# Kernel optimization log

Hardware: AMD Instinct MI355X
Metric: run time of the kernel (lower is better)

The kernel has to match this reference:

```python
import jax, jax.numpy as jnp
import numpy as np

EPS = 1e-8  # torch F.cosine_similarity default eps

N, M, PLANES = 4096, 4096, 512


def setup_inputs() -> dict:
    key = jax.random.key(0)
    k1, k2, k3, k4 = jax.random.split(key, 4)
    pre = jax.random.normal(k1, (N, PLANES), dtype=jnp.float32)
    cur = jax.random.normal(k2, (M, PLANES), dtype=jnp.float32)
    adj = jax.random.uniform(k3, (N, M), dtype=jnp.float32)
    stdv = 1.0 / np.sqrt(PLANES)
    weight = jax.random.uniform(k4, (PLANES, PLANES), dtype=jnp.float32,
                                minval=-stdv, maxval=stdv)
    return {"pre": pre, "cur": cur, "adj": adj, "weight": weight}


def reference(pre, cur, adj, weight):
    # --- GraphConvolution ---
    pre_w = pre @ weight            # [N, P]
    cur_w = cur @ weight            # [M, P]
    pre_h = adj @ cur_w             # [N, P]  adj_norm @ cur_
    cur_h = adj.T @ pre_w           # [M, P]  adj_t_norm @ pre_

    # --- edge_update: tan(cosine_similarity) for all (i, j) pairs, fused ---
    # cosine_similarity(x, y) = (x . y) / (max(||x||, eps) * max(||y||, eps))
    pre_norm = jnp.maximum(jnp.linalg.norm(pre_h, axis=1, keepdims=True), EPS)
    cur_norm = jnp.maximum(jnp.linalg.norm(cur_h, axis=1, keepdims=True), EPS)
    pre_n = pre_h / pre_norm        # [N, P]
    cur_n = cur_h / cur_norm        # [M, P]
    cos = pre_n @ cur_n.T           # [N, M]
    adj_out = jnp.tan(cos)          # [N, M]
    score = adj_out.reshape(-1)     # [N*M], row-major == i * M + j ordering
    return (score, adj_out)
```

## Files before the change

### kernel.cpp

```cpp
#include <hip/hip_runtime.h>

typedef unsigned short ushort_t;
typedef __attribute__((ext_vector_type(8))) short short8;
typedef __attribute__((ext_vector_type(4))) float f32x4;

__device__ __forceinline__ ushort_t f2bf(float x) {
  union { float f; unsigned u; } v; v.f = x;
  unsigned r = v.u + 0x7fffu + ((v.u >> 16) & 1u);
  return (ushort_t)(r >> 16);
}
__device__ __forceinline__ float bf2f(ushort_t h) {
  union { unsigned u; float f; } v; v.u = ((unsigned)h) << 16;
  return v.f;
}

__device__ __forceinline__ void async_cp16(const ushort_t* g, ushort_t* lds) {
  __builtin_amdgcn_global_load_lds(
      (const __attribute__((address_space(1))) unsigned int*)g,
      (__attribute__((address_space(3))) unsigned int*)lds, 16, 0, 0);
}

template <int MT, int NT, int BKT, int EPI>
__device__ __forceinline__ void gemm_core2(
    const ushort_t* __restrict__ A, int lda,
    const ushort_t* __restrict__ B, int ldb,
    int K,
    ushort_t* sA, ushort_t* sB,
    ushort_t* Cb, float* Cf0, float* Cf1, int ldc,
    const float* __restrict__ ip, const float* __restrict__ ic) {
  constexpr int MI = MT / 32, NI = NT / 32, KU = BKT / 32;
  constexpr int LPR = BKT / 8;
  constexpr int RPC = 256 / LPR;
  constexpr int ASZ = MT * BKT, BSZ = NT * BKT;
  static_assert(LPR == 8, "swizzle assumes 8 segs per row");
  static_assert(RPC % 8 == 0, "row&7 must be per-lane constant");
  const int t = threadIdx.x;
  const int wave = t >> 6, lane = t & 63;
  const int lm = lane & 15, lq = lane >> 4;
  const int wr = wave >> 1, wc = wave & 1;

  f32x4 acc[MI][NI] = {};

  const int srow = t / LPR;
  const int gseg = (t % LPR) ^ (srow & 7);
  const ushort_t* ga = A + (size_t)srow * lda + gseg * 8;
  const ushort_t* gb = B + (size_t)srow * ldb + gseg * 8;
  const int sw = lm & 7;

  auto stage = [&](int k0, int buf) {
    ushort_t* dA = sA + buf * ASZ + wave * 512;
    ushort_t* dB = sB + buf * BSZ + wave * 512;
#pragma unroll
    for (int j = 0; j < MT / RPC; j++)
      async_cp16(ga + k0 + (size_t)j * RPC * lda, dA + j * 2048);
#pragma unroll
    for (int j = 0; j < NT / RPC; j++)
      async_cp16(gb + k0 + (size_t)j * RPC * ldb, dB + j * 2048);
  };

  stage(0, 0);
  int cur = 0;
  for (int k0 = 0; k0 < K; k0 += BKT) {
    __syncthreads();
    if (k0 + BKT < K) stage(k0 + BKT, cur ^ 1);
    const ushort_t* cA = sA + cur * ASZ;
    const ushort_t* cB = sB + cur * BSZ;
#pragma unroll
    for (int ku = 0; ku < KU; ku++) {
      short8 af[MI], bf4[NI];
#pragma unroll
      for (int i = 0; i < MI; i++)
        af[i] = *(const short8*)(cA + (wr * (MT / 2) + i * 16 + lm) * BKT +
                                 ((ku * 4 + lq) ^ sw) * 8);
#pragma unroll
      for (int i = 0; i < NI; i++)
        bf4[i] = *(const short8*)(cB + (wc * (NT / 2) + i * 16 + lm) * BKT +
                                  ((ku * 4 + lq) ^ sw) * 8);
#pragma unroll
      for (int mt = 0; mt < MI; mt++)
#pragma unroll
        for (int nt = 0; nt < NI; nt++)
          acc[mt][nt] = __builtin_amdgcn_mfma_f32_16x16x32_bf16(
              af[mt], bf4[nt], acc[mt][nt], 0, 0, 0);
    }
    cur ^= 1;
  }

#pragma unroll
  for (int mt = 0; mt < MI; mt++) {
    int rb = wr * (MT / 2) + mt * 16 + lq * 4;
#pragma unroll
    for (int nt = 0; nt < NI; nt++) {
      int c = wc * (NT / 2) + nt * 16 + lm;
#pragma unroll
      for (int r = 0; r < 4; r++) {
        size_t idx = (size_t)(rb + r) * ldc + c;
        if (EPI == 1) {
          Cb[idx] = f2bf(acc[mt][nt][r]);
        } else {
          float v = __tanf(acc[mt][nt][r] * ip[rb + r] * ic[c]);
          Cf0[idx] = v;
          Cf1[idx] = v;
        }
      }
    }
  }
}

__global__ __launch_bounds__(256) void convT(
    const float* __restrict__ in, ushort_t* __restrict__ outn,
    ushort_t* __restrict__ outt, int n) {
  __shared__ float tile[64][65];
  const int t = threadIdx.x;
  const int r0 = blockIdx.y * 64, c0 = blockIdx.x * 64;
  const int cr = t >> 4;
  const int cc = (t & 15) * 4;
#pragma unroll
  for (int p = 0; p < 4; p++) {
    int r = cr + p * 16;
    float4 v = *(const float4*)(in + (size_t)(r0 + r) * n + c0 + cc);
    tile[r][cc + 0] = v.x; tile[r][cc + 1] = v.y;
    tile[r][cc + 2] = v.z; tile[r][cc + 3] = v.w;
    ushort4 o;
    o.x = f2bf(v.x); o.y = f2bf(v.y); o.z = f2bf(v.z); o.w = f2bf(v.w);
    *(ushort4*)(outn + (size_t)(r0 + r) * n + c0 + cc) = o;
  }
  __syncthreads();
#pragma unroll
  for (int p = 0; p < 4; p++) {
    int r = cr + p * 16;
    ushort4 o;
    o.x = f2bf(tile[cc + 0][r]); o.y = f2bf(tile[cc + 1][r]);
    o.z = f2bf(tile[cc + 2][r]); o.w = f2bf(tile[cc + 3][r]);
    *(ushort4*)(outt + (size_t)(c0 + r) * n + r0 + cc) = o;
  }
}

__global__ __launch_bounds__(256) void xcvt(
    const float* __restrict__ pre, const float* __restrict__ cur,
    ushort_t* __restrict__ xbf) {
  const size_t i = ((size_t)blockIdx.x * 256 + threadIdx.x) * 8;
  const float* src =
      (i < (size_t)4096 * 512) ? (pre + i) : (cur + (i - (size_t)4096 * 512));
  float4 a = *(const float4*)(src);
  float4 b = *(const float4*)(src + 4);
  short8 o;
  o[0] = (short)f2bf(a.x); o[1] = (short)f2bf(a.y);
  o[2] = (short)f2bf(a.z); o[3] = (short)f2bf(a.w);
  o[4] = (short)f2bf(b.x); o[5] = (short)f2bf(b.y);
  o[6] = (short)f2bf(b.z); o[7] = (short)f2bf(b.w);
  *(short8*)(xbf + i) = o;
}

__global__ __launch_bounds__(256) void k1_gemm(
    const ushort_t* __restrict__ wt_t, const ushort_t* __restrict__ xbf,
    ushort_t* __restrict__ pw_t) {
  __shared__ __align__(16) ushort_t sA[2 * 64 * 64];
  __shared__ __align__(16) ushort_t sB[2 * 128 * 64];
  const int bm = blockIdx.x & 7, bn = blockIdx.x >> 3;
  const ushort_t* A = wt_t + (size_t)bm * 64 * 512;
  const ushort_t* B = xbf + (size_t)bn * 128 * 512;
  ushort_t* C = pw_t + (size_t)bm * 64 * 8192 + bn * 128;
  gemm_core2<64, 128, 64, 1>(A, 512, B, 512, 512, sA, sB, C, nullptr, nullptr,
                             8192, nullptr, nullptr);
}

__global__ __launch_bounds__(256) void k2_gemm(
    const ushort_t* __restrict__ adj, const ushort_t* __restrict__ adj_t,
    const ushort_t* __restrict__ pw_t, ushort_t* __restrict__ pn) {
  __shared__ __align__(16) ushort_t sA[2 * 128 * 64];
  __shared__ __align__(16) ushort_t sB[2 * 64 * 64];
  const int b = blockIdx.x;
  const int xcd = b & 7, i = b >> 3;
  const int half = xcd & 1;
  const int bm = ((xcd >> 1) << 3) | (i & 7);
  const int bn = i >> 3;
  const ushort_t* A = (half ? adj_t : adj) + (size_t)bm * 128 * 4096;
  const ushort_t* B = pw_t + (size_t)bn * 64 * 8192 + (half ? 0 : 4096);
  ushort_t* C = pn + (half ? (size_t)4096 * 512 : 0) +
                (size_t)bm * 128 * 512 + bn * 64;
  gemm_core2<128, 64, 64, 1>(A, 4096, B, 8192, 4096, sA, sB, C, nullptr,
                             nullptr, 512, nullptr, nullptr);
}

__global__ __launch_bounds__(256) void invnorm_kernel(
    const ushort_t* __restrict__ pn, float* __restrict__ invn) {
  const int t = threadIdx.x;
  const int wave = t >> 6, lane = t & 63;
  const size_t row = (size_t)blockIdx.x * 4 + wave;
  const ushort_t* p = pn + row * 512 + lane * 8;
  short8 v = *(const short8*)p;
  float s = 0.f;
#pragma unroll
  for (int i = 0; i < 8; i++) {
    float f = bf2f((ushort_t)v[i]);
    s += f * f;
  }
#pragma unroll
  for (int off = 32; off > 0; off >>= 1) s += __shfl_xor(s, off, 64);
  if (lane == 0) invn[row] = 1.0f / fmaxf(sqrtf(s), 1e-8f);
}

__global__ __launch_bounds__(256) void k3_gemm(
    const ushort_t* __restrict__ pn, const float* __restrict__ invn,
    float* __restrict__ out) {
  __shared__ __align__(16) ushort_t sA[2 * 128 * 64];
  __shared__ __align__(16) ushort_t sB[2 * 128 * 64];
  const int bm = blockIdx.x & 31, bn = blockIdx.x >> 5;
  const ushort_t* A = pn + (size_t)bm * 128 * 512;
  const ushort_t* B = pn + (size_t)4096 * 512 + (size_t)bn * 128 * 512;
  float* C0 = out + (size_t)bm * 128 * 4096 + bn * 128;
  gemm_core2<128, 128, 64, 2>(A, 512, B, 512, 512, sA, sB, nullptr, C0,
                              C0 + (size_t)4096 * 4096, 4096,
                              invn + bm * 128, invn + 4096 + bn * 128);
}

extern "C" void kernel_launch(void* const* d_in, const int* in_sizes, int n_in,
                              void* d_out, int out_size, void* d_ws,
                              size_t ws_size, hipStream_t stream) {
  const float* pre = (const float*)d_in[0];
  const float* cur = (const float*)d_in[1];
  const float* adj = (const float*)d_in[2];
  const float* wt  = (const float*)d_in[3];
  float* out = (float*)d_out;

  ushort_t* adj_bf = (ushort_t*)d_ws;
  ushort_t* adj_t  = adj_bf + (size_t)4096 * 4096;
  ushort_t* pw_t   = adj_t + (size_t)4096 * 4096;
  ushort_t* pn     = pw_t + (size_t)512 * 8192;
  ushort_t* wt_t   = pn + (size_t)8192 * 512;
  ushort_t* wt_bf  = wt_t + (size_t)512 * 512;
  float*    invn   = (float*)(wt_bf + (size_t)512 * 512);
  ushort_t* xbf    = (ushort_t*)(invn + 8192);

  convT<<<dim3(64, 64), 256, 0, stream>>>(adj, adj_bf, adj_t, 4096);
  convT<<<dim3(8, 8), 256, 0, stream>>>(wt, wt_bf, wt_t, 512);
  xcvt<<<2048, 256, 0, stream>>>(pre, cur, xbf);
  k1_gemm<<<512, 256, 0, stream>>>(wt_t, xbf, pw_t);
  k2_gemm<<<512, 256, 0, stream>>>(adj_bf, adj_t, pw_t, pn);
  invnorm_kernel<<<2048, 256, 0, stream>>>(pn, invn);
  k3_gemm<<<1024, 256, 0, stream>>>(pn, invn, out);
}
```

Baseline: 311.5 us.

## Use triple-buffered LDS pipeline with single barrier per k-step in GEMMs

Result: no change. 305.8 us (-1.8%).

```diff
diff --git a/kernel.cpp b/kernel.cpp
--- a/kernel.cpp
+++ b/kernel.cpp
@@ -18,6 +18,101 @@
   __builtin_amdgcn_global_load_lds(
       (const __attribute__((address_space(1))) unsigned int*)g,
       (__attribute__((address_space(3))) unsigned int*)lds, 16, 0, 0);
+}
+
+template <int MT, int NT, int BKT, int EPI>
+__device__ __forceinline__ void gemm_core3(
+    const ushort_t* __restrict__ A, int lda,
+    const ushort_t* __restrict__ B, int ldb,
+    int K,
+    ushort_t* sA, ushort_t* sB,
+    ushort_t* Cb, float* Cf0, float* Cf1, int ldc,
+    const float* __restrict__ ip, const float* __restrict__ ic) {
+  constexpr int MI = MT / 32, NI = NT / 32, KU = BKT / 32;
+  constexpr int LPR = BKT / 8;
+  constexpr int RPC = 256 / LPR;
+  constexpr int ASZ = MT * BKT, BSZ = NT * BKT;
+  static_assert(LPR == 8, "swizzle assumes 8 segs per row");
+  static_assert(RPC % 8 == 0, "row&7 must be per-lane constant");
+  static_assert(MT / RPC + NT / RPC == 6, "vmcnt(6) assumes 6 loads/stage");
+  const int t = threadIdx.x;
+  const int wave = t >> 6, lane = t & 63;
+  const int lm = lane & 15, lq = lane >> 4;
+  const int wr = wave >> 1, wc = wave & 1;
+
+  f32x4 acc[MI][NI] = {};
+
+  const int srow = t / LPR;
+  const int gseg = (t % LPR) ^ (srow & 7);
+  const ushort_t* ga = A + (size_t)srow * lda + gseg * 8;
+  const ushort_t* gb = B + (size_t)srow * ldb + gseg * 8;
+  const int sw = lm & 7;
+
+  auto stage = [&](int k0, int buf) {
+    ushort_t* dA = sA + buf * ASZ + wave * 512;
+    ushort_t* dB = sB + buf * BSZ + wave * 512;
+#pragma unroll
+    for (int j = 0; j < MT / RPC; j++)
+      async_cp16(ga + k0 + (size_t)j * RPC * lda, dA + j * 2048);
+#pragma unroll
+    for (int j = 0; j < NT / RPC; j++)
+      async_cp16(gb + k0 + (size_t)j * RPC * ldb, dB + j * 2048);
+  };
+
+  const int NSTEP = K / BKT;
+  stage(0, 0);
+  int cur = 0, nxt = 1;
+  for (int s = 0; s < NSTEP; ++s) {
+    if (s + 1 < NSTEP) {
+      stage((s + 1) * BKT, nxt);
+      asm volatile("s_waitcnt vmcnt(6)" ::: "memory");
+    } else {
+      asm volatile("s_waitcnt vmcnt(0)" ::: "memory");
+    }
+    __builtin_amdgcn_s_barrier();
+    const ushort_t* cA = sA + cur * ASZ;
+    const ushort_t* cB = sB + cur * BSZ;
+#pragma unroll
+    for (int ku = 0; ku < KU; ku++) {
+      short8 af[MI], bf4[NI];
+#pragma unroll
+      for (int i = 0; i < MI; i++)
+        af[i] = *(const short8*)(cA + (wr * (MT / 2) + i * 16 + lm) * BKT +
+                                 ((ku * 4 + lq) ^ sw) * 8);
+#pragma unroll
+      for (int i = 0; i < NI; i++)
+        bf4[i] = *(const short8*)(cB + (wc * (NT / 2) + i * 16 + lm) * BKT +
+                                  ((ku * 4 + lq) ^ sw) * 8);
+#pragma unroll
+      for (int mt = 0; mt < MI; mt++)
+#pragma unroll
+        for (int nt = 0; nt < NI; nt++)
+          acc[mt][nt] = __builtin_amdgcn_mfma_f32_16x16x32_bf16(
+              af[mt], bf4[nt], acc[mt][nt], 0, 0, 0);
+    }
+    cur = nxt;
+    nxt = (nxt == 2) ? 0 : nxt + 1;
+  }
+
+#pragma unroll
+  for (int mt = 0; mt < MI; mt++) {
+    int rb = wr * (MT / 2) + mt * 16 + lq * 4;
+#pragma unroll
+    for (int nt = 0; nt < NI; nt++) {
+      int c = wc * (NT / 2) + nt * 16 + lm;
+#pragma unroll
+      for (int r = 0; r < 4; r++) {
+        size_t idx = (size_t)(rb + r) * ldc + c;
+        if (EPI == 1) {
+          Cb[idx] = f2bf(acc[mt][nt][r]);
+        } else {
+          float v = __tanf(acc[mt][nt][r] * ip[rb + r] * ic[c]);
+          Cf0[idx] = v;
+          Cf1[idx] = v;
+        }
+      }
+    }
+  }
 }
 
 template <int MT, int NT, int BKT, int EPI>
@@ -155,21 +250,21 @@
 __global__ __launch_bounds__(256) void k1_gemm(
     const ushort_t* __restrict__ wt_t, const ushort_t* __restrict__ xbf,
     ushort_t* __restrict__ pw_t) {
-  __shared__ __align__(16) ushort_t sA[2 * 64 * 64];
-  __shared__ __align__(16) ushort_t sB[2 * 128 * 64];
+  __shared__ __align__(16) ushort_t sA[3 * 64 * 64];
+  __shared__ __align__(16) ushort_t sB[3 * 128 * 64];
   const int bm = blockIdx.x & 7, bn = blockIdx.x >> 3;
   const ushort_t* A = wt_t + (size_t)bm * 64 * 512;
   const ushort_t* B = xbf + (size_t)bn * 128 * 512;
   ushort_t* C = pw_t + (size_t)bm * 64 * 8192 + bn * 128;
-  gemm_core2<64, 128, 64, 1>(A, 512, B, 512, 512, sA, sB, C, nullptr, nullptr,
+  gemm_core3<64, 128, 64, 1>(A, 512, B, 512, 512, sA, sB, C, nullptr, nullptr,
                              8192, nullptr, nullptr);
 }
 
 __global__ __launch_bounds__(256) void k2_gemm(
     const ushort_t* __restrict__ adj, const ushort_t* __restrict__ adj_t,
     const ushort_t* __restrict__ pw_t, ushort_t* __restrict__ pn) {
-  __shared__ __align__(16) ushort_t sA[2 * 128 * 64];
-  __shared__ __align__(16) ushort_t sB[2 * 64 * 64];
+  __shared__ __align__(16) ushort_t sA[3 * 128 * 64];
+  __shared__ __align__(16) ushort_t sB[3 * 64 * 64];
   const int b = blockIdx.x;
   const int xcd = b & 7, i = b >> 3;
   const int half = xcd & 1;
@@ -179,7 +274,7 @@
   const ushort_t* B = pw_t + (size_t)bn * 64 * 8192 + (half ? 0 : 4096);
   ushort_t* C = pn + (half ? (size_t)4096 * 512 : 0) +
                 (size_t)bm * 128 * 512 + bn * 64;
-  gemm_core2<128, 64, 64, 1>(A, 4096, B, 8192, 4096, sA, sB, C, nullptr,
+  gemm_core3<128, 64, 64, 1>(A, 4096, B, 8192, 4096, sA, sB, C, nullptr,
                              nullptr, 512, nullptr, nullptr);
 }
 
```
